# Kernel tuning notes

Measured on AMD Instinct MI355X. Metric: run time of the kernel, lower is better.

The kernel has to match this reference:

```python
import jax, jax.numpy as jnp
import numpy as np

N_NODES = 100000
N_EDGES = 640000
IN_DIM = 128
# PyG SAGEConv pyramid per SageCox(num_layers=4)
DIMS = [128, 85, 56, 28, 1]  # 85=int(128*2/3), 56=int(85*2/3), 28=int(56/2)


def setup_inputs() -> dict:
    key = jax.random.key(0)
    ks = jax.random.split(key, 2 + 3 * 4)
    inp = {
        "x": jax.random.normal(ks[0], (N_NODES, IN_DIM), dtype=jnp.float32),
        "edge_index": jax.random.randint(ks[1], (2, N_EDGES), 0, N_NODES, dtype=jnp.int64),
    }
    # Per-layer params: lin_l (weight+bias, applied to aggregated neighbors),
    # lin_r (weight only, applied to root features) -- PyG SAGEConv defaults.
    for i in range(4):
        din, dout = DIMS[i], DIMS[i + 1]
        inp[f"Wl{i}"] = jax.random.normal(ks[2 + 3 * i], (din, dout), dtype=jnp.float32) * 0.05
        inp[f"bl{i}"] = jax.random.normal(ks[3 + 3 * i], (dout,), dtype=jnp.float32) * 0.05
        inp[f"Wr{i}"] = jax.random.normal(ks[4 + 3 * i], (din, dout), dtype=jnp.float32) * 0.05
    return inp


def _sage_layer(x, src, dst, Wl, bl, Wr):
    # mean aggregation of source-node features at destination nodes
    msg = x[src]                                            # [E, din] gather
    agg = jax.ops.segment_sum(msg, dst, num_segments=N_NODES)
    deg = jax.ops.segment_sum(jnp.ones((src.shape[0],), x.dtype), dst,
                              num_segments=N_NODES)
    mean = agg / jnp.maximum(deg, 1.0)[:, None]             # [N, din]
    return mean @ Wl + bl + x @ Wr                          # [N, dout]


def reference(x, edge_index, Wl0, bl0, Wr0, Wl1, bl1, Wr1, Wl2, bl2, Wr2, Wl3, bl3, Wr3):
    src, dst = edge_index[0], edge_index[1]
    params = [(Wl0, bl0, Wr0), (Wl1, bl1, Wr1), (Wl2, bl2, Wr2), (Wl3, bl3, Wr3)]
    for Wl, bl, Wr in params:
        x = _sage_layer(x, src, dst, Wl, bl, Wr)
    return x  # [N, 1] risk scores
```

## Files before the change

### kernel.cpp

```cpp
#include <hip/hip_runtime.h>


#define NNODES 100000
#define NEDGES 640000

using bf16x8 = __attribute__((ext_vector_type(8))) short;
using f32x4  = __attribute__((ext_vector_type(4))) float;

__device__ __forceinline__ unsigned short f2bf(float f) {
    union { float f; unsigned u; } v; v.f = f;
    unsigned r = v.u + 0x7fffu + ((v.u >> 16) & 1u);
    return (unsigned short)(r >> 16);
}
__device__ __forceinline__ float bf2f(unsigned b) {
    union { unsigned u; float f; } v; v.u = b << 16;
    return v.f;
}


__global__ void hist_kernel(const int* __restrict__ edst, int* __restrict__ deg, int E) {
    int i = blockIdx.x * blockDim.x + threadIdx.x;
    if (i < E) atomicAdd(&deg[edst[i]], 1);
}

__global__ void scanA_kernel(const int* __restrict__ deg, int* __restrict__ bsum, int N) {
    __shared__ int s[256];
    int i = blockIdx.x * 256 + threadIdx.x;
    s[threadIdx.x] = (i < N) ? deg[i] : 0;
    __syncthreads();
    for (int off = 128; off > 0; off >>= 1) {
        if (threadIdx.x < off) s[threadIdx.x] += s[threadIdx.x + off];
        __syncthreads();
    }
    if (threadIdx.x == 0) bsum[blockIdx.x] = s[0];
}

__global__ void scanB_kernel(const int* __restrict__ bsum, int* __restrict__ bpre, int nb) {
    __shared__ int s[512];
    int t = threadIdx.x;
    int v = (t < nb) ? bsum[t] : 0;
    s[t] = v;
    __syncthreads();
    for (int off = 1; off < 512; off <<= 1) {
        int add = (t >= off) ? s[t - off] : 0;
        __syncthreads();
        s[t] += add;
        __syncthreads();
    }
    if (t < nb) bpre[t] = s[t] - v;
}

__global__ void scanC_kernel(const int* __restrict__ deg, const int* __restrict__ bpre,
                             int* __restrict__ rowptr, int* __restrict__ cursor, int N, int E) {
    __shared__ int s[256];
    int t = threadIdx.x;
    int i = blockIdx.x * 256 + t;
    int v = (i < N) ? deg[i] : 0;
    s[t] = v;
    __syncthreads();
    for (int off = 1; off < 256; off <<= 1) {
        int add = (t >= off) ? s[t - off] : 0;
        __syncthreads();
        s[t] += add;
        __syncthreads();
    }
    if (i < N) {
        int excl = bpre[blockIdx.x] + s[t] - v;
        rowptr[i] = excl;
        cursor[i] = excl;
        if (i == N - 1) rowptr[N] = E;
    }
}

__global__ void fill_kernel(const int* __restrict__ esrc, const int* __restrict__ edst,
                            int* __restrict__ cursor, int* __restrict__ csr, int E) {
    int i = blockIdx.x * blockDim.x + threadIdx.x;
    if (i < E) {
        int pos = atomicAdd(&cursor[edst[i]], 1);
        csr[pos] = esrc[i];
    }
}


__device__ __forceinline__ void packT_one(const float* Wl, const float* Wr,
                                          unsigned short* WcT, int idx, int DIN,
                                          int KP, int DOUT, int DOUTP) {
    int c = idx / KP, k = idx - c * KP;
    float v = 0.0f;
    if (k < DIN) {
        if (c < DOUT) v = Wl[k * DOUT + c];
        else if (c >= DOUTP && c < DOUTP + DOUT) v = Wr[k * DOUT + (c - DOUTP)];
    }
    WcT[idx] = f2bf(v);
}

__global__ void packAll_kernel(const float* __restrict__ Wl0, const float* __restrict__ Wr0,
                               const float* __restrict__ Wl1, const float* __restrict__ Wr1,
                               const float* __restrict__ Wl2, const float* __restrict__ Wr2,
                               unsigned short* __restrict__ Wc0,
                               unsigned short* __restrict__ Wc1,
                               unsigned short* __restrict__ Wc2) {
    const int S0 = 192 * 128, S1 = 128 * 96, S2 = 64 * 64;
    int idx = blockIdx.x * blockDim.x + threadIdx.x;
    if (idx < S0) packT_one(Wl0, Wr0, Wc0, idx, 128, 128, 85, 96);
    else if (idx < S0 + S1) packT_one(Wl1, Wr1, Wc1, idx - S0, 85, 96, 56, 64);
    else if (idx < S0 + S1 + S2) packT_one(Wl2, Wr2, Wc2, idx - S0 - S1, 56, 64, 28, 32);
}


template <bool XFP32, int KP, int SIN, int NTILES, int DOUT, int SPP>
__global__ void __launch_bounds__(256)
projm_kernel(const void* __restrict__ xin,
             const unsigned short* __restrict__ WcT,
             const float* __restrict__ bl,
             unsigned short* __restrict__ p,
             unsigned short* __restrict__ acc_out, int N) {
    constexpr int KT   = KP / 32;
    constexpr int HT   = NTILES / 2;
    constexpr int WSTR = KP + 8;
    constexpr int LSTR = SPP + 8;
    static_assert(HT * 16 == SPP, "phase width must equal SPP");
    __shared__ short wS[HT * 16 * WSTR];
    __shared__ short oS[128 * LSTR];

    const int lane = threadIdx.x & 63;
    const int wave = threadIdx.x >> 6;
    const int l15 = lane & 15;
    const int lk  = lane >> 4;
    const int row0 = blockIdx.x * 128;
    const int wrow = wave * 32;

    auto stageW = [&](int colbase) {
        for (int c8 = threadIdx.x; c8 < HT * 16 * (KP / 8); c8 += 256) {
            const int c  = c8 / (KP / 8);
            const int k8 = c8 - c * (KP / 8);
            *(bf16x8*)(wS + c * WSTR + k8 * 8) =
                *(const bf16x8*)(WcT + (size_t)(colbase + c) * KP + k8 * 8);
        }
    };

    stageW(0);

    bf16x8 afrag[2][KT];
#pragma unroll
    for (int h = 0; h < 2; ++h) {
        int arow = row0 + wrow + h * 16 + l15;
        if (arow >= N) arow = N - 1;
        if constexpr (XFP32) {
            const float* xr = (const float*)xin + (size_t)arow * SIN + lk * 8;
#pragma unroll
            for (int kt = 0; kt < KT; ++kt) {
                const float4 a = *(const float4*)(xr + kt * 32);
                const float4 b = *(const float4*)(xr + kt * 32 + 4);
                bf16x8 v;
                v[0] = (short)f2bf(a.x); v[1] = (short)f2bf(a.y);
                v[2] = (short)f2bf(a.z); v[3] = (short)f2bf(a.w);
                v[4] = (short)f2bf(b.x); v[5] = (short)f2bf(b.y);
                v[6] = (short)f2bf(b.z); v[7] = (short)f2bf(b.w);
                afrag[h][kt] = v;
            }
        } else {
            const unsigned short* xr = (const unsigned short*)xin + (size_t)arow * SIN + lk * 8;
#pragma unroll
            for (int kt = 0; kt < KT; ++kt)
                afrag[h][kt] = *(const bf16x8*)(xr + kt * 32);
        }
    }

    __syncthreads();

    const int rows_here = min(128, N - row0);
    const int cnt8 = rows_here * (SPP / 8);

    auto computePhase = [&](bool withBias) {
#pragma unroll 2
        for (int nt = 0; nt < HT; ++nt) {
            const short* wp = wS + (size_t)(nt * 16 + l15) * WSTR + lk * 8;
            bf16x8 bfrag[KT];
#pragma unroll
            for (int kt = 0; kt < KT; ++kt)
                bfrag[kt] = *(const bf16x8*)(wp + kt * 32);

            f32x4 a0 = {0.f, 0.f, 0.f, 0.f};
            f32x4 a1 = {0.f, 0.f, 0.f, 0.f};
#pragma unroll
            for (int kt = 0; kt < KT; ++kt) {
                a0 = __builtin_amdgcn_mfma_f32_16x16x32_bf16(afrag[0][kt], bfrag[kt], a0, 0, 0, 0);
                a1 = __builtin_amdgcn_mfma_f32_16x16x32_bf16(afrag[1][kt], bfrag[kt], a1, 0, 0, 0);
            }

            const int co = nt * 16 + l15;
            const float bias = (withBias && co < DOUT) ? bl[co] : 0.0f;
#pragma unroll
            for (int h = 0; h < 2; ++h) {
                const f32x4 a = h ? a1 : a0;
                const int rl = wrow + h * 16 + lk * 4;
#pragma unroll
                for (int j = 0; j < 4; ++j)
                    oS[(rl + j) * LSTR + co] = (short)f2bf(a[j] + bias);
            }
        }
    };

    auto storeOut = [&](unsigned short* dst) {
        for (int e8 = threadIdx.x; e8 < cnt8; e8 += 256) {
            const int row = e8 / (SPP / 8);
            const int c8  = e8 - row * (SPP / 8);
            *(bf16x8*)(dst + (size_t)row0 * SPP + (size_t)e8 * 8) =
                *(const bf16x8*)(oS + row * LSTR + c8 * 8);
        }
    };

    computePhase(false);
    __syncthreads();
    storeOut(p);
    stageW(HT * 16);
    __syncthreads();
    computePhase(true);
    __syncthreads();
    storeOut(acc_out);
}


template <int DOUT, int SP, int SN, int NPW>
__global__ void __launch_bounds__(256)
gatherb_kernel(const int* __restrict__ rowptr, const int* __restrict__ csr,
               const unsigned short* __restrict__ p, const unsigned short* __restrict__ acc,
               unsigned short* __restrict__ xnext, int N) {
    const int wid  = (blockIdx.x * 256 + threadIdx.x) >> 6;
    const int lane = threadIdx.x & 63;
    int node, hl;
    if constexpr (NPW == 1) {
        node = __builtin_amdgcn_readfirstlane(wid);
        hl = lane;
    } else {
        node = wid * 2 + (lane >> 5);
        hl = lane & 31;
    }
    if (node >= N) return;
    const int beg = rowptr[node], end = rowptr[node + 1];
    const float inv = 1.0f / (float)max(end - beg, 1);
    constexpr int NPAIR = (DOUT + 1) / 2;
    const int co = 2 * hl;

    float s0 = 0.f, s1 = 0.f, s2 = 0.f, s3 = 0.f;
    float h0 = 0.f, h1 = 0.f, h2 = 0.f, h3 = 0.f;
    if (hl < NPAIR) {
        int j = beg;
        for (; j + 4 <= end; j += 4) {
            const unsigned u0 = *(const unsigned*)(p + (size_t)csr[j]     * SP + co);
            const unsigned u1 = *(const unsigned*)(p + (size_t)csr[j + 1] * SP + co);
            const unsigned u2 = *(const unsigned*)(p + (size_t)csr[j + 2] * SP + co);
            const unsigned u3 = *(const unsigned*)(p + (size_t)csr[j + 3] * SP + co);
            s0 += bf2f(u0 & 0xffffu); h0 += bf2f(u0 >> 16);
            s1 += bf2f(u1 & 0xffffu); h1 += bf2f(u1 >> 16);
            s2 += bf2f(u2 & 0xffffu); h2 += bf2f(u2 >> 16);
            s3 += bf2f(u3 & 0xffffu); h3 += bf2f(u3 >> 16);
        }
        for (; j < end; ++j) {
            const unsigned u0 = *(const unsigned*)(p + (size_t)csr[j] * SP + co);
            s0 += bf2f(u0 & 0xffffu); h0 += bf2f(u0 >> 16);
        }
    }
    if (co < SN) {
        const float slo = (s0 + s1) + (s2 + s3);
        const float shi = (h0 + h1) + (h2 + h3);
        float lo = 0.f, hi = 0.f;
        if (co < DOUT)     lo = bf2f((unsigned)acc[(size_t)node * SP + co])     + inv * slo;
        if (co + 1 < DOUT) hi = bf2f((unsigned)acc[(size_t)node * SP + co + 1]) + inv * shi;
        const unsigned w = (unsigned)f2bf(lo) | ((unsigned)f2bf(hi) << 16);
        *(unsigned*)(xnext + (size_t)node * SN + co) = w;
    }
}


__global__ void __launch_bounds__(256)
gather2g_kernel(const int* __restrict__ rowptr, const int* __restrict__ csr,
                const unsigned short* __restrict__ p, const unsigned short* __restrict__ acc,
                const float* __restrict__ Wl3, const float* __restrict__ bl3,
                const float* __restrict__ Wr3,
                float* __restrict__ p3, float* __restrict__ out, int N) {
    const int wid  = (blockIdx.x * 256 + threadIdx.x) >> 6;
    const int lane = threadIdx.x & 63;
    const int node = wid * 2 + (lane >> 5);
    const int hl   = lane & 31;
    if (node >= N) return;
    const int beg = rowptr[node], end = rowptr[node + 1];
    const float inv = 1.0f / (float)max(end - beg, 1);
    const int co = 2 * hl;

    float s0 = 0.f, s1 = 0.f, s2 = 0.f, s3 = 0.f;
    float h0 = 0.f, h1 = 0.f, h2 = 0.f, h3 = 0.f;
    if (hl < 14) {
        int j = beg;
        for (; j + 4 <= end; j += 4) {
            const unsigned u0 = *(const unsigned*)(p + (size_t)csr[j]     * 32 + co);
            const unsigned u1 = *(const unsigned*)(p + (size_t)csr[j + 1] * 32 + co);
            const unsigned u2 = *(const unsigned*)(p + (size_t)csr[j + 2] * 32 + co);
            const unsigned u3 = *(const unsigned*)(p + (size_t)csr[j + 3] * 32 + co);
            s0 += bf2f(u0 & 0xffffu); h0 += bf2f(u0 >> 16);
            s1 += bf2f(u1 & 0xffffu); h1 += bf2f(u1 >> 16);
            s2 += bf2f(u2 & 0xffffu); h2 += bf2f(u2 >> 16);
            s3 += bf2f(u3 & 0xffffu); h3 += bf2f(u3 >> 16);
        }
        for (; j < end; ++j) {
            const unsigned u0 = *(const unsigned*)(p + (size_t)csr[j] * 32 + co);
            s0 += bf2f(u0 & 0xffffu); h0 += bf2f(u0 >> 16);
        }
    }
    float xlo = 0.f, xhi = 0.f, wl0 = 0.f, wl1 = 0.f, wr0 = 0.f, wr1 = 0.f;
    if (hl < 14) {
        xlo = bf2f((unsigned)acc[(size_t)node * 32 + co])     + inv * ((s0 + s1) + (s2 + s3));
        xhi = bf2f((unsigned)acc[(size_t)node * 32 + co + 1]) + inv * ((h0 + h1) + (h2 + h3));
        wl0 = Wl3[co]; wl1 = Wl3[co + 1];
        wr0 = Wr3[co]; wr1 = Wr3[co + 1];
    }
    float sl = xlo * wl0 + xhi * wl1;
    float sr = xlo * wr0 + xhi * wr1;
#pragma unroll
    for (int off = 16; off > 0; off >>= 1) {
        sl += __shfl_xor(sl, off, 64);
        sr += __shfl_xor(sr, off, 64);
    }
    if (hl == 0) {
        p3[node] = sl;
        out[node] = sr + bl3[0];
    }
}

__global__ void gather1_kernel(const int* __restrict__ rowptr, const int* __restrict__ csr,
                               const float* __restrict__ p, float* __restrict__ out, int N) {
    const int node = blockIdx.x * blockDim.x + threadIdx.x;
    if (node >= N) return;
    const int beg = rowptr[node], end = rowptr[node + 1];
    const float inv = 1.0f / (float)max(end - beg, 1);
    float a0 = 0.f, a1 = 0.f, a2 = 0.f, a3 = 0.f;
    int j = beg;
    for (; j + 4 <= end; j += 4) {
        a0 += p[csr[j]]; a1 += p[csr[j + 1]]; a2 += p[csr[j + 2]]; a3 += p[csr[j + 3]];
    }
    for (; j < end; ++j) a0 += p[csr[j]];
    out[node] += inv * ((a0 + a1) + (a2 + a3));
}


extern "C" void kernel_launch(void* const* d_in, const int* in_sizes, int n_in,
                              void* d_out, int out_size, void* d_ws, size_t ws_size,
                              hipStream_t stream) {
    const float* x  = (const float*)d_in[0];
    const int*   ei = (const int*)d_in[1];
    const int N = NNODES;
    const int E = NEDGES;
    const int* esrc = ei;
    const int* edst = ei + E;

    const float* Wl[4] = {(const float*)d_in[2], (const float*)d_in[5],
                          (const float*)d_in[8], (const float*)d_in[11]};
    const float* bl[4] = {(const float*)d_in[3], (const float*)d_in[6],
                          (const float*)d_in[9], (const float*)d_in[12]};
    const float* Wr[4] = {(const float*)d_in[4], (const float*)d_in[7],
                          (const float*)d_in[10], (const float*)d_in[13]};

    char* base = (char*)d_ws;
    size_t off = 0;
    auto alloc = [&](size_t bytes) {
        char* r = base + off;
        off += (bytes + 255) & ~(size_t)255;
        return r;
    };
    unsigned short* pB   = (unsigned short*)alloc((size_t)N * 96 * 2);
    unsigned short* accB = (unsigned short*)alloc((size_t)N * 96 * 2);
    unsigned short* xp   = (unsigned short*)alloc((size_t)N * 96 * 2);
    float*          p3   = (float*)alloc((size_t)N * 4);
    unsigned short* Wc0  = (unsigned short*)alloc((size_t)192 * 128 * 2);
    unsigned short* Wc1  = (unsigned short*)alloc((size_t)128 * 96 * 2);
    unsigned short* Wc2  = (unsigned short*)alloc((size_t)64 * 64 * 2);
    int* degi   = (int*)alloc((size_t)N * 4);
    int* rowptr = (int*)alloc((size_t)(N + 1) * 4);
    int* cursor = (int*)alloc((size_t)N * 4);
    int* csr    = (int*)alloc((size_t)E * 4);
    int* bsum   = (int*)alloc(512 * 4);
    int* bpre   = (int*)alloc(512 * 4);

    unsigned short* x2 = xp;

    const int nb = (N + 255) / 256;

    hipMemsetAsync(degi, 0, (size_t)N * sizeof(int), stream);
    hist_kernel<<<(E + 255) / 256, 256, 0, stream>>>(edst, degi, E);
    scanA_kernel<<<nb, 256, 0, stream>>>(degi, bsum, N);
    scanB_kernel<<<1, 512, 0, stream>>>(bsum, bpre, nb);
    scanC_kernel<<<nb, 256, 0, stream>>>(degi, bpre, rowptr, cursor, N, E);
    fill_kernel<<<(E + 255) / 256, 256, 0, stream>>>(esrc, edst, cursor, csr, E);

    const int packTot = 192 * 128 + 128 * 96 + 64 * 64;
    packAll_kernel<<<(packTot + 255) / 256, 256, 0, stream>>>(
        Wl[0], Wr[0], Wl[1], Wr[1], Wl[2], Wr[2], Wc0, Wc1, Wc2);

    const int projBlocks = (N + 127) / 128;

    projm_kernel<true, 128, 128, 12, 85, 96><<<projBlocks, 256, 0, stream>>>(
        x, Wc0, bl[0], pB, accB, N);
    gatherb_kernel<85, 96, 96, 1><<<(N + 3) / 4, 256, 0, stream>>>(
        rowptr, csr, pB, accB, xp, N);

    projm_kernel<false, 96, 96, 8, 56, 64><<<projBlocks, 256, 0, stream>>>(
        xp, Wc1, bl[1], pB, accB, N);
    gatherb_kernel<56, 64, 64, 2><<<(N + 7) / 8, 256, 0, stream>>>(
        rowptr, csr, pB, accB, x2, N);

    projm_kernel<false, 64, 64, 4, 28, 32><<<projBlocks, 256, 0, stream>>>(
        x2, Wc2, bl[2], pB, accB, N);

    gather2g_kernel<<<(N + 7) / 8, 256, 0, stream>>>(
        rowptr, csr, pB, accB, Wl[3], bl[3], Wr[3], p3, (float*)d_out, N);
    gather1_kernel<<<(N + 255) / 256, 256, 0, stream>>>(
        rowptr, csr, p3, (float*)d_out, N);
}
```

Baseline: 233.9 us.

## Fuse weight packing with histogram, drop scanB, partition CSR fill by destination range

Weight packing and the degree histogram now run as one launch split by block index. The middle single-block scan kernel is removed, and each scanC block instead reduces the preceding block sums itself. The CSR fill becomes a grid-stride kernel in which each of 8 block groups handles only one destination range, aiming to localize atomics and writes. In exchange, every fill block scans all edges, so the edst array is read eight times in total.

```diff
diff --git a/kernel.cpp b/kernel.cpp
--- a/kernel.cpp
+++ b/kernel.cpp
@@ -15,70 +15,6 @@
 __device__ __forceinline__ float bf2f(unsigned b) {
     union { unsigned u; float f; } v; v.u = b << 16;
     return v.f;
-}
-
-
-__global__ void hist_kernel(const int* __restrict__ edst, int* __restrict__ deg, int E) {
-    int i = blockIdx.x * blockDim.x + threadIdx.x;
-    if (i < E) atomicAdd(&deg[edst[i]], 1);
-}
-
-__global__ void scanA_kernel(const int* __restrict__ deg, int* __restrict__ bsum, int N) {
-    __shared__ int s[256];
-    int i = blockIdx.x * 256 + threadIdx.x;
-    s[threadIdx.x] = (i < N) ? deg[i] : 0;
-    __syncthreads();
-    for (int off = 128; off > 0; off >>= 1) {
-        if (threadIdx.x < off) s[threadIdx.x] += s[threadIdx.x + off];
-        __syncthreads();
-    }
-    if (threadIdx.x == 0) bsum[blockIdx.x] = s[0];
-}
-
-__global__ void scanB_kernel(const int* __restrict__ bsum, int* __restrict__ bpre, int nb) {
-    __shared__ int s[512];
-    int t = threadIdx.x;
-    int v = (t < nb) ? bsum[t] : 0;
-    s[t] = v;
-    __syncthreads();
-    for (int off = 1; off < 512; off <<= 1) {
-        int add = (t >= off) ? s[t - off] : 0;
-        __syncthreads();
-        s[t] += add;
-        __syncthreads();
-    }
-    if (t < nb) bpre[t] = s[t] - v;
-}
-
-__global__ void scanC_kernel(const int* __restrict__ deg, const int* __restrict__ bpre,
-                             int* __restrict__ rowptr, int* __restrict__ cursor, int N, int E) {
-    __shared__ int s[256];
-    int t = threadIdx.x;
-    int i = blockIdx.x * 256 + t;
-    int v = (i < N) ? deg[i] : 0;
-    s[t] = v;
-    __syncthreads();
-    for (int off = 1; off < 256; off <<= 1) {
-        int add = (t >= off) ? s[t - off] : 0;
-        __syncthreads();
-        s[t] += add;
-        __syncthreads();
-    }
-    if (i < N) {
-        int excl = bpre[blockIdx.x] + s[t] - v;
-        rowptr[i] = excl;
-        cursor[i] = excl;
-        if (i == N - 1) rowptr[N] = E;
-    }
-}
-
-__global__ void fill_kernel(const int* __restrict__ esrc, const int* __restrict__ edst,
-                            int* __restrict__ cursor, int* __restrict__ csr, int E) {
-    int i = blockIdx.x * blockDim.x + threadIdx.x;
-    if (i < E) {
-        int pos = atomicAdd(&cursor[edst[i]], 1);
-        csr[pos] = esrc[i];
-    }
 }
 
 
@@ -94,17 +30,91 @@
     WcT[idx] = f2bf(v);
 }
 
-__global__ void packAll_kernel(const float* __restrict__ Wl0, const float* __restrict__ Wr0,
-                               const float* __restrict__ Wl1, const float* __restrict__ Wr1,
-                               const float* __restrict__ Wl2, const float* __restrict__ Wr2,
-                               unsigned short* __restrict__ Wc0,
-                               unsigned short* __restrict__ Wc1,
-                               unsigned short* __restrict__ Wc2) {
+
+#define PACKB 160
+
+__global__ void packhist_kernel(const float* __restrict__ Wl0, const float* __restrict__ Wr0,
+                                const float* __restrict__ Wl1, const float* __restrict__ Wr1,
+                                const float* __restrict__ Wl2, const float* __restrict__ Wr2,
+                                unsigned short* __restrict__ Wc0,
+                                unsigned short* __restrict__ Wc1,
+                                unsigned short* __restrict__ Wc2,
+                                const int* __restrict__ edst, int* __restrict__ deg, int E) {
     const int S0 = 192 * 128, S1 = 128 * 96, S2 = 64 * 64;
-    int idx = blockIdx.x * blockDim.x + threadIdx.x;
-    if (idx < S0) packT_one(Wl0, Wr0, Wc0, idx, 128, 128, 85, 96);
-    else if (idx < S0 + S1) packT_one(Wl1, Wr1, Wc1, idx - S0, 85, 96, 56, 64);
-    else if (idx < S0 + S1 + S2) packT_one(Wl2, Wr2, Wc2, idx - S0 - S1, 56, 64, 28, 32);
+    if (blockIdx.x < PACKB) {
+        int idx = blockIdx.x * 256 + threadIdx.x;
+        if (idx < S0) packT_one(Wl0, Wr0, Wc0, idx, 128, 128, 85, 96);
+        else if (idx < S0 + S1) packT_one(Wl1, Wr1, Wc1, idx - S0, 85, 96, 56, 64);
+        else if (idx < S0 + S1 + S2) packT_one(Wl2, Wr2, Wc2, idx - S0 - S1, 56, 64, 28, 32);
+    } else {
+        int i = (blockIdx.x - PACKB) * 256 + threadIdx.x;
+        if (i < E) atomicAdd(&deg[edst[i]], 1);
+    }
+}
+
+
+__global__ void scanA_kernel(const int* __restrict__ deg, int* __restrict__ bsum, int N) {
+    __shared__ int s[256];
+    int i = blockIdx.x * 256 + threadIdx.x;
+    s[threadIdx.x] = (i < N) ? deg[i] : 0;
+    __syncthreads();
+    for (int off = 128; off > 0; off >>= 1) {
+        if (threadIdx.x < off) s[threadIdx.x] += s[threadIdx.x + off];
+        __syncthreads();
+    }
+    if (threadIdx.x == 0) bsum[blockIdx.x] = s[0];
+}
+
+__global__ void scanC_kernel(const int* __restrict__ deg, const int* __restrict__ bsum,
+                             int* __restrict__ rowptr, int* __restrict__ cursor, int N, int E) {
+    __shared__ int s[256];
+    int t = threadIdx.x;
+
+    int a = 0;
+    for (int j = t; j < blockIdx.x; j += 256) a += bsum[j];
+    s[t] = a;
+    __syncthreads();
+    for (int off = 128; off > 0; off >>= 1) {
+        if (t < off) s[t] += s[t + off];
+        __syncthreads();
+    }
+    const int base = s[0];
+    __syncthreads();
+
+    int i = blockIdx.x * 256 + t;
+    int v = (i < N) ? deg[i] : 0;
+    s[t] = v;
+    __syncthreads();
+    for (int off = 1; off < 256; off <<= 1) {
+        int add = (t >= off) ? s[t - off] : 0;
+        __syncthreads();
+        s[t] += add;
+        __syncthreads();
+    }
+    if (i < N) {
+        int excl = base + s[t] - v;
+        rowptr[i] = excl;
+        cursor[i] = excl;
+        if (i == N - 1) rowptr[N] = E;
+    }
+}
+
+
+__global__ void fillp_kernel(const int* __restrict__ esrc, const int* __restrict__ edst,
+                             int* __restrict__ cursor, int* __restrict__ csr, int E, int N) {
+    const int part = blockIdx.x & 7;
+    const int sub  = blockIdx.x >> 3;
+    const int nsub = gridDim.x >> 3;
+    const int chunk = N >> 3;
+    const int lo = part * chunk;
+    const int hi = (part == 7) ? N : lo + chunk;
+    for (int i = sub * 256 + threadIdx.x; i < E; i += nsub * 256) {
+        const int d = edst[i];
+        if (d >= lo && d < hi) {
+            int pos = atomicAdd(&cursor[d], 1);
+            csr[pos] = esrc[i];
+        }
+    }
 }
 
 
@@ -380,22 +390,19 @@
     int* cursor = (int*)alloc((size_t)N * 4);
     int* csr    = (int*)alloc((size_t)E * 4);
     int* bsum   = (int*)alloc(512 * 4);
-    int* bpre   = (int*)alloc(512 * 4);
 
     unsigned short* x2 = xp;
 
     const int nb = (N + 255) / 256;
+    const int histB = (E + 255) / 256;
 
     hipMemsetAsync(degi, 0, (size_t)N * sizeof(int), stream);
-    hist_kernel<<<(E + 255) / 256, 256, 0, stream>>>(edst, degi, E);
+    packhist_kernel<<<PACKB + histB, 256, 0, stream>>>(
+        Wl[0], Wr[0], Wl[1], Wr[1], Wl[2], Wr[2], Wc0, Wc1, Wc2, edst, degi, E);
+
     scanA_kernel<<<nb, 256, 0, stream>>>(degi, bsum, N);
-    scanB_kernel<<<1, 512, 0, stream>>>(bsum, bpre, nb);
-    scanC_kernel<<<nb, 256, 0, stream>>>(degi, bpre, rowptr, cursor, N, E);
-    fill_kernel<<<(E + 255) / 256, 256, 0, stream>>>(esrc, edst, cursor, csr, E);
-
-    const int packTot = 192 * 128 + 128 * 96 + 64 * 64;
-    packAll_kernel<<<(packTot + 255) / 256, 256, 0, stream>>>(
-        Wl[0], Wr[0], Wl[1], Wr[1], Wl[2], Wr[2], Wc0, Wc1, Wc2);
+    scanC_kernel<<<nb, 256, 0, stream>>>(degi, bsum, rowptr, cursor, N, E);
+    fillp_kernel<<<2048, 256, 0, stream>>>(esrc, edst, cursor, csr, E, N);
 
     const int projBlocks = (N + 127) / 128;
 
```

After: 222.1 us. -5.1%, faster.
